# Optimization experiments

Hardware: AMD Instinct MI355X
Metric: run time of the kernel (lower is better)

The kernel has to match this reference:

```python
import jax, jax.numpy as jnp
import numpy as np

V, E, H, TAG, B, S = 100000, 128, 256, 16, 64, 512
T = TAG + 2            # tag_size + start + end
START, END = T - 2, T - 1


def setup_inputs() -> dict:
    key = jax.random.key(0)
    ks = jax.random.split(key, 16)
    x = jax.random.randint(ks[0], (B, S), 0, V)
    lengths = jax.random.randint(ks[1], (B,), S // 2, S + 1)
    mask = (jnp.arange(S)[None, :] < lengths[:, None]).astype(jnp.int32)

    def rn(k, shape, s=0.05):
        return (jax.random.normal(k, shape) * s).astype(jnp.float32)

    embed = rn(ks[2], (V, E), 0.1)
    Wih_f = rn(ks[3], (4 * H, E)); Whh_f = rn(ks[4], (4 * H, H))
    bih_f = rn(ks[5], (4 * H,));   bhh_f = rn(ks[6], (4 * H,))
    Wih_b = rn(ks[7], (4 * H, E)); Whh_b = rn(ks[8], (4 * H, H))
    bih_b = rn(ks[9], (4 * H,));   bhh_b = rn(ks[10], (4 * H,))
    Wc = rn(ks[11], (T, 2 * H));   bc = rn(ks[12], (T,))
    trans = rn(ks[13], (T, T), 0.1)
    trans = trans.at[:, START].set(-1000.0).at[END, :].set(-1000.0)
    h0 = rn(ks[14], (2, B, H), 1.0)  # init_hidden uses randn
    c0 = rn(ks[15], (2, B, H), 1.0)
    return dict(x=x, mask=mask, embed=embed,
                Wih_f=Wih_f, Whh_f=Whh_f, bih_f=bih_f, bhh_f=bhh_f,
                Wih_b=Wih_b, Whh_b=Whh_b, bih_b=bih_b, bhh_b=bhh_b,
                Wc=Wc, bc=bc, trans=trans, h0=h0, c0=c0)


def _lstm_dir(xs, h0, c0, Wih, Whh, bih, bhh, reverse):
    # xs: [S,B,E]; PyTorch gate order i,f,g,o
    xp = jnp.einsum('sbe,ge->sbg', xs, Wih) + bih  # batch the input GEMM

    def step(carry, xg):
        h, c = carry
        g = xg + h @ Whh.T + bhh
        i, f, gg, o = jnp.split(g, 4, axis=-1)
        c = jax.nn.sigmoid(f) * c + jax.nn.sigmoid(i) * jnp.tanh(gg)
        h = jax.nn.sigmoid(o) * jnp.tanh(c)
        return (h, c), h

    _, hs = jax.lax.scan(step, (h0, c0), xp, reverse=reverse)
    return hs  # [S,B,H]


def _viterbi(feats, mask, trans):
    # feats [B,S,T]; scores[t,b,prev,cur] = feats[t,b,cur] + trans[prev,cur]
    scores = feats.transpose(1, 0, 2)[:, :, None, :] + trans[None, None, :, :]  # [S,B,T,T]
    mT = mask.T  # [S,B]
    partition0 = scores[0, :, START, :]  # [B,T]

    def step(partition, inp):
        sc_t, m_t = inp
        cur = sc_t + partition[:, :, None]        # add over prev-tag axis
        new_p = jnp.max(cur, axis=1)
        bp = jnp.argmax(cur, axis=1).astype(jnp.int32)
        bp = jnp.where(m_t[:, None] > 0, bp, 0)   # zero back-pointers at pad
        return new_p, (new_p, bp)

    _, (parts, bps) = jax.lax.scan(step, partition0, (scores[1:], mT[1:]))
    part_hist = jnp.concatenate([partition0[None], parts], axis=0)  # [S,B,T]

    lengths = jnp.sum(mask, axis=1)
    last_pos = lengths - 1  # [B]
    ph_b = part_hist.transpose(1, 0, 2)  # [B,S,T]
    last_part = jnp.take_along_axis(ph_b, last_pos[:, None, None], axis=1)[:, 0, :]  # [B,T]
    last_vals = last_part[:, :, None] + trans[None]
    max_value = jnp.max(last_vals, axis=1)                    # [B,T]
    last_bp = jnp.argmax(last_vals, axis=1).astype(jnp.int32)
    pointer = last_bp[:, END]                                  # [B]

    back = jnp.concatenate([bps, jnp.zeros((1, B, T), jnp.int32)], axis=0)  # [S,B,T]
    bp_b = back.transpose(1, 0, 2)  # [B,S,T]
    bp_b = bp_b.at[jnp.arange(B), last_pos].set(pointer[:, None])  # insert_last scatter
    back = bp_b.transpose(1, 0, 2)

    def trace(ptr, bp_t):
        new = jnp.take_along_axis(bp_t, ptr[:, None], axis=1)[:, 0]
        return new, new

    _, dec = jax.lax.scan(trace, pointer, back[:-1], reverse=True)  # [S-1,B]
    decode = jnp.concatenate([dec, pointer[None]], axis=0).T        # [B,S]
    path_score = max_value[:, END]
    return path_score, decode


def reference(x, mask, embed, Wih_f, Whh_f, bih_f, bhh_f,
              Wih_b, Whh_b, bih_b, bhh_b, Wc, bc, trans, h0, c0):
    xs = embed[x].transpose(1, 0, 2)  # [S,B,E]
    hf = _lstm_dir(xs, h0[0], c0[0], Wih_f, Whh_f, bih_f, bhh_f, False)
    hb = _lstm_dir(xs, h0[1], c0[1], Wih_b, Whh_b, bih_b, bhh_b, True)
    out = jnp.concatenate([hf, hb], axis=-1)            # [S,B,2H]
    feats = (out @ Wc.T + bc).transpose(1, 0, 2)        # [B,S,T]
    return _viterbi(feats, mask, trans)
```

## Files before the change

### kernel.cpp

```cpp
#include <hip/hip_runtime.h>

#define SLEN 512
#define BATCH 64
#define HID 256
#define EMB 128
#define NT 18
#define NCHAIN 128
#define FB 8
#define SB 4

typedef unsigned int u32;

__device__ __forceinline__ float sigmoidf_(float v) { return 1.0f / (1.0f + expf(-v)); }
__device__ __forceinline__ u32 aload(const u32* p) {
  return __hip_atomic_load((u32*)p, __ATOMIC_RELAXED, __HIP_MEMORY_SCOPE_AGENT);
}

__global__ __launch_bounds__(512, 2) void lstm_kernel(
    const int* __restrict__ x, const float* __restrict__ embed,
    const float* __restrict__ Wih_f, const float* __restrict__ Whh_f,
    const float* __restrict__ bih_f, const float* __restrict__ bhh_f,
    const float* __restrict__ Wih_b, const float* __restrict__ Whh_b,
    const float* __restrict__ bih_b, const float* __restrict__ bhh_b,
    const float* __restrict__ h0, const float* __restrict__ c0,
    float* __restrict__ h_hist, u32* __restrict__ flags)
{
  const int rk   = blockIdx.x >> 6;
  const int q    = blockIdx.x & 63;
  const int dir  = q >> 5;
  const int bA   = (q & 31) * 2, bB = bA + 1;
  const int chA  = dir * BATCH + bA, chB = chA + 1;
  const int tid  = threadIdx.x;
  const int row  = tid & 255;
  const int kh   = tid >> 8;
  const int gi   = row >> 6;
  const int uo   = row & 63;
  const int grow = gi * 256 + rk * 64 + uo;
  const int wv   = tid >> 6;
  const int lane = tid & 63;

  const float* Wih = dir ? Wih_b : Wih_f;
  const float* Whh = dir ? Whh_b : Whh_f;
  const float* bih = dir ? bih_b : bih_f;
  const float* bhh = dir ? bhh_b : bhh_f;

  float4 wreg[48];
  if (kh == 0) {
#pragma unroll
    for (int c = 0; c < 48; ++c)
      wreg[c] = *(const float4*)(Whh + (size_t)grow * 256 + c * 4);
  } else {
#pragma unroll
    for (int c = 0; c < 16; ++c)
      wreg[c] = *(const float4*)(Whh + (size_t)grow * 256 + 192 + c * 4);
#pragma unroll
    for (int c = 0; c < 32; ++c)
      wreg[16 + c] = *(const float4*)(Wih + (size_t)grow * 128 + c * 4);
  }
  const int vb = kh ? 192 : 0;

  __shared__ float vA[384], vB[384];
  __shared__ float redA[2][256], redB[2][256];

  float bias4[4] = {0, 0, 0, 0};
  float creg = 0.0f;
  if (wv >= 6) {
    int b = (wv == 6) ? bA : bB;
#pragma unroll
    for (int gg = 0; gg < 4; ++gg) {
      int rr = gg * 256 + rk * 64 + lane;
      bias4[gg] = bih[rr] + bhh[rr];
    }
    creg = c0[(size_t)(dir * BATCH + b) * HID + rk * 64 + lane];
  }

  auto TS = [&](int s) { s = s < SLEN ? s : SLEN - 1; return dir ? (SLEN - 1 - s) : s; };

  const int ee = tid - 256;
  float evA = 0.0f, evB = 0.0f;
  int xvA = 0, xvB = 0;

  if (tid < 256) {
    vA[tid] = h0[(size_t)(dir * BATCH + bA) * HID + tid];
    vB[tid] = h0[(size_t)(dir * BATCH + bB) * HID + tid];
  } else if (tid < 384) {
    vA[256 + ee] = embed[(size_t)x[bA * SLEN + TS(0)] * EMB + ee];
    evA = embed[(size_t)x[bA * SLEN + TS(1)] * EMB + ee];
    xvA = x[bA * SLEN + TS(2)];
    evB = embed[(size_t)x[bB * SLEN + TS(0)] * EMB + ee];
    xvB = x[bB * SLEN + TS(1)];
  }
  __syncthreads();

  for (int it = 0; it < SLEN; ++it) {
    const int t = dir ? (SLEN - 1 - it) : it;

    {
      float acc = 0.0f;
#pragma unroll
      for (int c = 0; c < 48; ++c) {
        float4 w4 = wreg[c];
        float4 v4 = *(const float4*)&vA[vb + c * 4];
        acc = fmaf(w4.x, v4.x, acc); acc = fmaf(w4.y, v4.y, acc);
        acc = fmaf(w4.z, v4.z, acc); acc = fmaf(w4.w, v4.w, acc);
      }
      redA[kh][row] = acc;
    }
    __syncthreads();

    if (wv == 6) {
      float s0 = bias4[0] + redA[0][lane]       + redA[1][lane];
      float s1 = bias4[1] + redA[0][64 + lane]  + redA[1][64 + lane];
      float s2 = bias4[2] + redA[0][128 + lane] + redA[1][128 + lane];
      float s3 = bias4[3] + redA[0][192 + lane] + redA[1][192 + lane];
      float ig = sigmoidf_(s0), fg = sigmoidf_(s1);
      float gv = tanhf(s2),     og = sigmoidf_(s3);
      creg = fg * creg + ig * gv;
      float hv = og * tanhf(creg);
      __hip_atomic_store(h_hist + ((size_t)(dir * SLEN + t) * BATCH + bA) * HID
                           + rk * 64 + lane,
                         hv, __ATOMIC_RELAXED, __HIP_MEMORY_SCOPE_AGENT);
      asm volatile("s_waitcnt vmcnt(0)" ::: "memory");
      if (lane == 0)
        __hip_atomic_store(flags + ((size_t)chA * SLEN + it) * 4 + rk, 1u,
                           __ATOMIC_RELAXED, __HIP_MEMORY_SCOPE_AGENT);
    } else if (wv < 4) {
      if (it > 0) {
        const u32* fp = flags + ((size_t)chB * SLEN + (it - 1)) * 4 + wv;
        u32 v = aload(fp); int sp = 0;
        while (!__all(v != 0) && ++sp < (1 << 14)) {
          __builtin_amdgcn_s_sleep(1);
          v = aload(fp);
        }
        asm volatile("" ::: "memory");
        const int tp = dir ? (t + 1) : (t - 1);
        u32 hw = aload((const u32*)(h_hist +
                    ((size_t)(dir * SLEN + tp) * BATCH + bB) * HID) + tid);
        *(u32*)&vB[tid] = hw;
      }
    } else if (wv < 6) {
      vB[256 + ee] = evB;
      evB = embed[(size_t)xvB * EMB + ee];
      xvB = x[bB * SLEN + TS(it + 2)];
    }
    __syncthreads();

    {
      float acc = 0.0f;
#pragma unroll
      for (int c = 0; c < 48; ++c) {
        float4 w4 = wreg[c];
        float4 v4 = *(const float4*)&vB[vb + c * 4];
        acc = fmaf(w4.x, v4.x, acc); acc = fmaf(w4.y, v4.y, acc);
        acc = fmaf(w4.z, v4.z, acc); acc = fmaf(w4.w, v4.w, acc);
      }
      redB[kh][row] = acc;
    }
    __syncthreads();

    if (wv == 7) {
      float s0 = bias4[0] + redB[0][lane]       + redB[1][lane];
      float s1 = bias4[1] + redB[0][64 + lane]  + redB[1][64 + lane];
      float s2 = bias4[2] + redB[0][128 + lane] + redB[1][128 + lane];
      float s3 = bias4[3] + redB[0][192 + lane] + redB[1][192 + lane];
      float ig = sigmoidf_(s0), fg = sigmoidf_(s1);
      float gv = tanhf(s2),     og = sigmoidf_(s3);
      creg = fg * creg + ig * gv;
      float hv = og * tanhf(creg);
      __hip_atomic_store(h_hist + ((size_t)(dir * SLEN + t) * BATCH + bB) * HID
                           + rk * 64 + lane,
                         hv, __ATOMIC_RELAXED, __HIP_MEMORY_SCOPE_AGENT);
      asm volatile("s_waitcnt vmcnt(0)" ::: "memory");
      if (lane == 0)
        __hip_atomic_store(flags + ((size_t)chB * SLEN + it) * 4 + rk, 1u,
                           __ATOMIC_RELAXED, __HIP_MEMORY_SCOPE_AGENT);
    } else if (wv < 4) {
      if (it < SLEN - 1) {
        const u32* fp = flags + ((size_t)chA * SLEN + it) * 4 + wv;
        u32 v = aload(fp); int sp = 0;
        while (!__all(v != 0) && ++sp < (1 << 14)) {
          __builtin_amdgcn_s_sleep(1);
          v = aload(fp);
        }
        asm volatile("" ::: "memory");
        u32 hw = aload((const u32*)(h_hist +
                    ((size_t)(dir * SLEN + t) * BATCH + bA) * HID) + tid);
        *(u32*)&vA[tid] = hw;
      }
    } else if (wv < 6) {
      if (it < SLEN - 1) {
        vA[256 + ee] = evA;
        evA = embed[(size_t)xvA * EMB + ee];
        xvA = x[bA * SLEN + TS(it + 3)];
      }
    }
    __syncthreads();
  }
}

__global__ __launch_bounds__(256) void feats_kernel(
    const float* __restrict__ h_hist, const float* __restrict__ Wc,
    const float* __restrict__ bc, float* __restrict__ feats)
{
  const int s0  = (blockIdx.x >> 3) * SB;
  const int b0  = (blockIdx.x & 7) * FB;
  const int tid = threadIdx.x;
  __shared__ float wc[NT * 516];
  __shared__ float hl[FB * 516];
  __shared__ float bcl[NT];
  if (tid < NT) bcl[tid] = bc[tid];
  for (int f = tid * 4; f < NT * 512; f += 1024) {
    float4 v = *(const float4*)(Wc + f);
    *(float4*)&wc[(f >> 9) * 516 + (f & 511)] = v;
  }
  for (int si = 0; si < SB; ++si) {
    const int s = s0 + si;
    const float* src0 = h_hist + ((size_t)s * BATCH + b0) * HID;
    const float* src1 = h_hist + ((size_t)(SLEN + s) * BATCH + b0) * HID;
    for (int f = tid * 4; f < FB * 256; f += 1024) {
      int b = f >> 8, j = f & 255;
      *(float4*)&hl[b * 516 + j]       = *(const float4*)(src0 + f);
      *(float4*)&hl[b * 516 + 256 + j] = *(const float4*)(src1 + f);
    }
    __syncthreads();
    if (tid < FB * NT) {
      int b = tid / NT, tag = tid - b * NT;
      float a = bcl[tag];
      const float* hp = &hl[b * 516];
      const float* wp = &wc[tag * 516];
#pragma unroll 8
      for (int k = 0; k < 512; k += 4) {
        float4 h4 = *(const float4*)(hp + k);
        float4 w4 = *(const float4*)(wp + k);
        a = fmaf(h4.x, w4.x, a); a = fmaf(h4.y, w4.y, a);
        a = fmaf(h4.z, w4.z, a); a = fmaf(h4.w, w4.w, a);
      }
      feats[((size_t)s * BATCH + b0 + b) * NT + tag] = a;
    }
    __syncthreads();
  }
}

__global__ __launch_bounds__(64) void viterbi_kernel(
    const float* __restrict__ feats, const int* __restrict__ mask,
    const float* __restrict__ trans, float* __restrict__ out)
{
  const int b = blockIdx.x;
  const int lane = threadIdx.x;
  __shared__ float tr[NT][NT + 1];
  __shared__ float part[2][NT + 2];
  __shared__ float lastp[NT + 2];
  __shared__ unsigned char bp[SLEN][20];
  __shared__ int len_s;

  for (int f = lane; f < NT * NT; f += 64) tr[f / NT][f % NT] = trans[f];
  int m = 0;
#pragma unroll
  for (int i = 0; i < 8; ++i) m += mask[b * SLEN + lane * 8 + i];
  for (int off = 32; off; off >>= 1) m += __shfl_down(m, off);
  if (lane == 0) len_s = m;
  __syncthreads();
  const int len = len_s;

  if (lane < NT) part[0][lane] = feats[(size_t)b * NT + lane] + tr[16][lane];
  __syncthreads();

  int cur = 0;
  float fnext = (lane < NT) ? feats[((size_t)BATCH + b) * NT + lane] : 0.0f;
  int   mnext = mask[b * SLEN + 1];
  for (int t = 1; t < SLEN; ++t) {
    float fcur = fnext; int mcur = mnext;
    if (t < SLEN - 1) {
      fnext = (lane < NT) ? feats[((size_t)(t + 1) * BATCH + b) * NT + lane] : 0.0f;
      mnext = mask[b * SLEN + t + 1];
    }
    if (lane < NT) {
      float best = -3.0e38f; int bf = 0;
#pragma unroll
      for (int from = 0; from < NT; ++from) {
        float v = (fcur + tr[from][lane]) + part[cur][from];
        if (v > best) { best = v; bf = from; }
      }
      part[cur ^ 1][lane] = best;
      bp[t][lane] = mcur ? (unsigned char)bf : (unsigned char)0;
      if (t == len - 1) lastp[lane] = best;
    }
    cur ^= 1;
    __syncthreads();
  }

  if (lane == 0) {
    float best = -3.0e38f; int bf = 0;
    for (int from = 0; from < NT; ++from) {
      float v = lastp[from] + tr[from][17];
      if (v > best) { best = v; bf = from; }
    }
    out[b] = best;
    int ptr = bf;
    out[BATCH + (size_t)b * SLEN + (SLEN - 1)] = (float)ptr;
    for (int i = SLEN - 2; i >= 0; --i) {
      int nw = (i == len - 1) ? bf : (int)bp[i + 1][ptr];
      out[BATCH + (size_t)b * SLEN + i] = (float)nw;
      ptr = nw;
    }
  }
}

extern "C" void kernel_launch(void* const* d_in, const int* in_sizes, int n_in,
                              void* d_out, int out_size, void* d_ws, size_t ws_size,
                              hipStream_t stream) {
  const int*   x      = (const int*)  d_in[0];
  const int*   mask   = (const int*)  d_in[1];
  const float* embed  = (const float*)d_in[2];
  const float* Wih_f  = (const float*)d_in[3];
  const float* Whh_f  = (const float*)d_in[4];
  const float* bih_f  = (const float*)d_in[5];
  const float* bhh_f  = (const float*)d_in[6];
  const float* Wih_b  = (const float*)d_in[7];
  const float* Whh_b  = (const float*)d_in[8];
  const float* bih_b  = (const float*)d_in[9];
  const float* bhh_b  = (const float*)d_in[10];
  const float* Wc     = (const float*)d_in[11];
  const float* bc     = (const float*)d_in[12];
  const float* trans  = (const float*)d_in[13];
  const float* h0     = (const float*)d_in[14];
  const float* c0     = (const float*)d_in[15];
  float* out = (float*)d_out;

  char* ws = (char*)d_ws;
  float* h_hist = (float*)ws;
  u32*   flags  = (u32*)(ws + (size_t)67108864);
  float* feats  = (float*)(ws + (size_t)67108864);

  hipMemsetAsync(flags, 0, (size_t)NCHAIN * SLEN * 4 * sizeof(u32), stream);
  lstm_kernel<<<256, 512, 0, stream>>>(x, embed, Wih_f, Whh_f, bih_f, bhh_f,
                                       Wih_b, Whh_b, bih_b, bhh_b, h0, c0,
                                       h_hist, flags);
  feats_kernel<<<(SLEN / SB) * 8, 256, 0, stream>>>(h_hist, Wc, bc, feats);
  viterbi_kernel<<<BATCH, 64, 0, stream>>>(feats, mask, trans, out);
}
```

Baseline: 2.072 ms.

## Split LSTM recurrent matvec across all waves and batch cross-block h polling

Each of the 8 waves now owns a 48-wide K slice and computes 4 gate rows per lane, replacing the old two-half K split. Partial sums go to an 8-way shared reduction. The waits for both chains' hidden-state flags are moved into one phase, so the B-chain value is prefetched into a register one phase early. __syncthreads is replaced with a raw s_barrier that uses explicit lgkmcnt waits and sched barriers. The goal is shorter per-step critical-path latency and fewer exposed spin-waits, at the cost of a larger reduction and a possibly longer stall in that single polling phase.

```diff
diff --git a/kernel.cpp b/kernel.cpp
--- a/kernel.cpp
+++ b/kernel.cpp
@@ -14,6 +14,12 @@
 __device__ __forceinline__ float sigmoidf_(float v) { return 1.0f / (1.0f + expf(-v)); }
 __device__ __forceinline__ u32 aload(const u32* p) {
   return __hip_atomic_load((u32*)p, __ATOMIC_RELAXED, __HIP_MEMORY_SCOPE_AGENT);
+}
+__device__ __forceinline__ void bar() {
+  __builtin_amdgcn_sched_barrier(0);
+  asm volatile("s_waitcnt lgkmcnt(0)" ::: "memory");
+  __builtin_amdgcn_s_barrier();
+  __builtin_amdgcn_sched_barrier(0);
 }
 
 __global__ __launch_bounds__(512, 2) void lstm_kernel(
@@ -31,46 +37,39 @@
   const int bA   = (q & 31) * 2, bB = bA + 1;
   const int chA  = dir * BATCH + bA, chB = chA + 1;
   const int tid  = threadIdx.x;
-  const int row  = tid & 255;
-  const int kh   = tid >> 8;
-  const int gi   = row >> 6;
-  const int uo   = row & 63;
-  const int grow = gi * 256 + rk * 64 + uo;
   const int wv   = tid >> 6;
   const int lane = tid & 63;
+  const int rb   = lane * 4;
+  const int gi   = rb >> 6;
+  const int grow0 = gi * 256 + rk * 64 + (rb & 63);
 
   const float* Wih = dir ? Wih_b : Wih_f;
   const float* Whh = dir ? Whh_b : Whh_f;
   const float* bih = dir ? bih_b : bih_f;
   const float* bhh = dir ? bhh_b : bhh_f;
 
-  float4 wreg[48];
-  if (kh == 0) {
-#pragma unroll
-    for (int c = 0; c < 48; ++c)
-      wreg[c] = *(const float4*)(Whh + (size_t)grow * 256 + c * 4);
-  } else {
-#pragma unroll
-    for (int c = 0; c < 16; ++c)
-      wreg[c] = *(const float4*)(Whh + (size_t)grow * 256 + 192 + c * 4);
-#pragma unroll
-    for (int c = 0; c < 32; ++c)
-      wreg[16 + c] = *(const float4*)(Wih + (size_t)grow * 128 + c * 4);
-  }
-  const int vb = kh ? 192 : 0;
+  float4 wreg[4][12];
+#pragma unroll
+  for (int i = 0; i < 4; ++i)
+#pragma unroll
+    for (int c = 0; c < 12; ++c) {
+      int k0 = wv * 48 + c * 4;
+      if (k0 < 256)
+        wreg[i][c] = *(const float4*)(Whh + (size_t)(grow0 + i) * 256 + k0);
+      else
+        wreg[i][c] = *(const float4*)(Wih + (size_t)(grow0 + i) * 128 + (k0 - 256));
+    }
 
   __shared__ float vA[384], vB[384];
-  __shared__ float redA[2][256], redB[2][256];
+  __shared__ float redA[8 * 256], redB[8 * 256];
 
   float bias4[4] = {0, 0, 0, 0};
   float creg = 0.0f;
   if (wv >= 6) {
     int b = (wv == 6) ? bA : bB;
 #pragma unroll
-    for (int gg = 0; gg < 4; ++gg) {
-      int rr = gg * 256 + rk * 64 + lane;
-      bias4[gg] = bih[rr] + bhh[rr];
-    }
+    for (int gg = 0; gg < 4; ++gg)
+      bias4[gg] = bih[gg * 256 + rk * 64 + lane] + bhh[gg * 256 + rk * 64 + lane];
     creg = c0[(size_t)(dir * BATCH + b) * HID + rk * 64 + lane];
   }
 
@@ -79,6 +78,7 @@
   const int ee = tid - 256;
   float evA = 0.0f, evB = 0.0f;
   int xvA = 0, xvB = 0;
+  u32 hwB = 0;
 
   if (tid < 256) {
     vA[tid] = h0[(size_t)(dir * BATCH + bA) * HID + tid];
@@ -94,25 +94,35 @@
 
   for (int it = 0; it < SLEN; ++it) {
     const int t = dir ? (SLEN - 1 - it) : it;
+    const int kb = wv * 48;
 
     {
-      float acc = 0.0f;
-#pragma unroll
-      for (int c = 0; c < 48; ++c) {
-        float4 w4 = wreg[c];
-        float4 v4 = *(const float4*)&vA[vb + c * 4];
-        acc = fmaf(w4.x, v4.x, acc); acc = fmaf(w4.y, v4.y, acc);
-        acc = fmaf(w4.z, v4.z, acc); acc = fmaf(w4.w, v4.w, acc);
-      }
-      redA[kh][row] = acc;
-    }
-    __syncthreads();
+      float4 acc = {0, 0, 0, 0};
+#pragma unroll
+      for (int c = 0; c < 12; ++c) {
+        float4 v4 = *(const float4*)&vA[kb + c * 4];
+        acc.x = fmaf(wreg[0][c].x, v4.x, acc.x); acc.x = fmaf(wreg[0][c].y, v4.y, acc.x);
+        acc.x = fmaf(wreg[0][c].z, v4.z, acc.x); acc.x = fmaf(wreg[0][c].w, v4.w, acc.x);
+        acc.y = fmaf(wreg[1][c].x, v4.x, acc.y); acc.y = fmaf(wreg[1][c].y, v4.y, acc.y);
+        acc.y = fmaf(wreg[1][c].z, v4.z, acc.y); acc.y = fmaf(wreg[1][c].w, v4.w, acc.y);
+        acc.z = fmaf(wreg[2][c].x, v4.x, acc.z); acc.z = fmaf(wreg[2][c].y, v4.y, acc.z);
+        acc.z = fmaf(wreg[2][c].z, v4.z, acc.z); acc.z = fmaf(wreg[2][c].w, v4.w, acc.z);
+        acc.w = fmaf(wreg[3][c].x, v4.x, acc.w); acc.w = fmaf(wreg[3][c].y, v4.y, acc.w);
+        acc.w = fmaf(wreg[3][c].z, v4.z, acc.w); acc.w = fmaf(wreg[3][c].w, v4.w, acc.w);
+      }
+      *(float4*)&redA[wv * 256 + rb] = acc;
+    }
+    bar();
 
     if (wv == 6) {
-      float s0 = bias4[0] + redA[0][lane]       + redA[1][lane];
-      float s1 = bias4[1] + redA[0][64 + lane]  + redA[1][64 + lane];
-      float s2 = bias4[2] + redA[0][128 + lane] + redA[1][128 + lane];
-      float s3 = bias4[3] + redA[0][192 + lane] + redA[1][192 + lane];
+      float s0 = bias4[0], s1 = bias4[1], s2 = bias4[2], s3 = bias4[3];
+#pragma unroll
+      for (int w = 0; w < 8; ++w) {
+        s0 += redA[w * 256 + lane];
+        s1 += redA[w * 256 + 64 + lane];
+        s2 += redA[w * 256 + 128 + lane];
+        s3 += redA[w * 256 + 192 + lane];
+      }
       float ig = sigmoidf_(s0), fg = sigmoidf_(s1);
       float gv = tanhf(s2),     og = sigmoidf_(s3);
       creg = fg * creg + ig * gv;
@@ -124,45 +134,42 @@
       if (lane == 0)
         __hip_atomic_store(flags + ((size_t)chA * SLEN + it) * 4 + rk, 1u,
                            __ATOMIC_RELAXED, __HIP_MEMORY_SCOPE_AGENT);
-    } else if (wv < 4) {
-      if (it > 0) {
-        const u32* fp = flags + ((size_t)chB * SLEN + (it - 1)) * 4 + wv;
-        u32 v = aload(fp); int sp = 0;
-        while (!__all(v != 0) && ++sp < (1 << 14)) {
-          __builtin_amdgcn_s_sleep(1);
-          v = aload(fp);
-        }
-        asm volatile("" ::: "memory");
-        const int tp = dir ? (t + 1) : (t - 1);
-        u32 hw = aload((const u32*)(h_hist +
-                    ((size_t)(dir * SLEN + tp) * BATCH + bB) * HID) + tid);
-        *(u32*)&vB[tid] = hw;
-      }
+    } else if (tid < 256) {
+      if (it > 0) *(u32*)&vB[tid] = hwB;
     } else if (wv < 6) {
       vB[256 + ee] = evB;
       evB = embed[(size_t)xvB * EMB + ee];
       xvB = x[bB * SLEN + TS(it + 2)];
     }
-    __syncthreads();
+    bar();
 
     {
-      float acc = 0.0f;
-#pragma unroll
-      for (int c = 0; c < 48; ++c) {
-        float4 w4 = wreg[c];
-        float4 v4 = *(const float4*)&vB[vb + c * 4];
-        acc = fmaf(w4.x, v4.x, acc); acc = fmaf(w4.y, v4.y, acc);
-        acc = fmaf(w4.z, v4.z, acc); acc = fmaf(w4.w, v4.w, acc);
-      }
-      redB[kh][row] = acc;
-    }
-    __syncthreads();
+      float4 acc = {0, 0, 0, 0};
+#pragma unroll
+      for (int c = 0; c < 12; ++c) {
+        float4 v4 = *(const float4*)&vB[kb + c * 4];
+        acc.x = fmaf(wreg[0][c].x, v4.x, acc.x); acc.x = fmaf(wreg[0][c].y, v4.y, acc.x);
+        acc.x = fmaf(wreg[0][c].z, v4.z, acc.x); acc.x = fmaf(wreg[0][c].w, v4.w, acc.x);
+        acc.y = fmaf(wreg[1][c].x, v4.x, acc.y); acc.y = fmaf(wreg[1][c].y, v4.y, acc.y);
+        acc.y = fmaf(wreg[1][c].z, v4.z, acc.y); acc.y = fmaf(wreg[1][c].w, v4.w, acc.y);
+        acc.z = fmaf(wreg[2][c].x, v4.x, acc.z); acc.z = fmaf(wreg[2][c].y, v4.y, acc.z);
+        acc.z = fmaf(wreg[2][c].z, v4.z, acc.z); acc.z = fmaf(wreg[2][c].w, v4.w, acc.z);
+        acc.w = fmaf(wreg[3][c].x, v4.x, acc.w); acc.w = fmaf(wreg[3][c].y, v4.y, acc.w);
+        acc.w = fmaf(wreg[3][c].z, v4.z, acc.w); acc.w = fmaf(wreg[3][c].w, v4.w, acc.w);
+      }
+      *(float4*)&redB[wv * 256 + rb] = acc;
+    }
+    bar();
 
     if (wv == 7) {
-      float s0 = bias4[0] + redB[0][lane]       + redB[1][lane];
-      float s1 = bias4[1] + redB[0][64 + lane]  + redB[1][64 + lane];
-      float s2 = bias4[2] + redB[0][128 + lane] + redB[1][128 + lane];
-      float s3 = bias4[3] + redB[0][192 + lane] + redB[1][192 + lane];
+      float s0 = bias4[0], s1 = bias4[1], s2 = bias4[2], s3 = bias4[3];
+#pragma unroll
+      for (int w = 0; w < 8; ++w) {
+        s0 += redB[w * 256 + lane];
+        s1 += redB[w * 256 + 64 + lane];
+        s2 += redB[w * 256 + 128 + lane];
+        s3 += redB[w * 256 + 192 + lane];
+      }
       float ig = sigmoidf_(s0), fg = sigmoidf_(s1);
       float gv = tanhf(s2),     og = sigmoidf_(s3);
       creg = fg * creg + ig * gv;
@@ -174,18 +181,21 @@
       if (lane == 0)
         __hip_atomic_store(flags + ((size_t)chB * SLEN + it) * 4 + rk, 1u,
                            __ATOMIC_RELAXED, __HIP_MEMORY_SCOPE_AGENT);
-    } else if (wv < 4) {
+    } else if (tid < 256) {
       if (it < SLEN - 1) {
-        const u32* fp = flags + ((size_t)chA * SLEN + it) * 4 + wv;
-        u32 v = aload(fp); int sp = 0;
-        while (!__all(v != 0) && ++sp < (1 << 14)) {
-          __builtin_amdgcn_s_sleep(1);
-          v = aload(fp);
-        }
+        const u32* fpA = flags + ((size_t)chA * SLEN + it) * 4 + wv;
+        u32 v = aload(fpA); int sp = 0;
+        while (v == 0 && ++sp < (1 << 14)) { __builtin_amdgcn_s_sleep(1); v = aload(fpA); }
         asm volatile("" ::: "memory");
-        u32 hw = aload((const u32*)(h_hist +
-                    ((size_t)(dir * SLEN + t) * BATCH + bA) * HID) + tid);
-        *(u32*)&vA[tid] = hw;
+        u32 ha = aload((const u32*)(h_hist +
+                   ((size_t)(dir * SLEN + t) * BATCH + bA) * HID) + tid);
+        *(u32*)&vA[tid] = ha;
+        const u32* fpB = flags + ((size_t)chB * SLEN + it) * 4 + wv;
+        v = aload(fpB); sp = 0;
+        while (v == 0 && ++sp < (1 << 14)) { __builtin_amdgcn_s_sleep(1); v = aload(fpB); }
+        asm volatile("" ::: "memory");
+        hwB = aload((const u32*)(h_hist +
+                 ((size_t)(dir * SLEN + t) * BATCH + bB) * HID) + tid);
       }
     } else if (wv < 6) {
       if (it < SLEN - 1) {
@@ -194,7 +204,7 @@
         xvA = x[bA * SLEN + TS(it + 3)];
       }
     }
-    __syncthreads();
+    bar();
   }
 }
 
```

After: 2.079 ms. About the same (+0.3%).
